# Kernel tuning notes

Measured on AMD Instinct MI355X. Metric: run time of the kernel, lower is better.

The kernel has to match this reference:

```python
import jax, jax.numpy as jnp
import numpy as np

N, D_IN, D_HID, D_Z = 8192, 512, 256, 64


def setup_inputs() -> dict:
    key = jax.random.key(0)
    k1, k2, k3, k4, k5 = jax.random.split(key, 5)
    x = jax.random.normal(k1, (N, D_IN), dtype=jnp.float32)
    adj = jax.random.uniform(k2, (N, N), dtype=jnp.float32)
    # Glorot-ish init for GCN weights
    W_hidden = jax.random.normal(k3, (D_IN, D_HID), dtype=jnp.float32) / np.sqrt(D_IN)
    W_mean = jax.random.normal(k4, (D_HID, D_Z), dtype=jnp.float32) / np.sqrt(D_HID)
    W_logstd = jax.random.normal(k5, (D_HID, D_Z), dtype=jnp.float32) / np.sqrt(D_HID)
    return {"x": x, "adj": adj, "W_hidden": W_hidden, "W_mean": W_mean, "W_logstd": W_logstd}


def _gcn(x, adj, W, act):
    # GraphConvolution (eval mode: dropout is identity): act(adj @ (x @ W))
    support = x @ W            # [N, out]
    out = adj @ support        # [N, out]  (sparse adj matmul in the original)
    return act(out)


def reference(x, adj, W_hidden, W_mean, W_logstd):
    hidden = _gcn(x, adj, W_hidden, jax.nn.relu)        # [N, hid]
    z_mean = _gcn(hidden, adj, W_mean, lambda t: t)     # [N, z]
    z_log_std = _gcn(hidden, adj, W_logstd, lambda t: t)
    # eval-mode reparameterize: z = z_mean
    z = z_mean
    # InnerProductDecoder with act = identity (as constructed in GCNModelVAE)
    recon = z @ z.T                                     # [N, N]
    return recon, z_mean, z_log_std
```

## Files before the change

### kernel.cpp

```cpp
#include <hip/hip_runtime.h>
#include <hip/hip_bf16.h>
#include <cstdint>


typedef __hip_bfloat16 hbf16;
typedef __bf16 bf16x8 __attribute__((ext_vector_type(8)));
typedef __bf16 bf16x4 __attribute__((ext_vector_type(4)));
typedef float  f32x4  __attribute__((ext_vector_type(4)));

#define N_NODES 8192
#define D_INF   512
#define D_HID   256
#define D_Z     64
#define KSPLIT  8

enum { EPI_NORM = 0, EPI_RELU = 1, EPI_TRANS = 2, EPI_SPLIT = 3 };

__device__ __forceinline__ float tofloat(float v) { return v; }
__device__ __forceinline__ float tofloat(hbf16 v) { return __bfloat162float(v); }

__device__ __forceinline__ bf16x8 load8(const hbf16* p) {
    return *(const bf16x8*)p;
}
__device__ __forceinline__ bf16x8 load8(const float* p) {
    f32x4 f0 = *(const f32x4*)p;
    f32x4 f1 = *(const f32x4*)(p + 4);
    bf16x8 r;
    r[0] = (__bf16)f0[0]; r[1] = (__bf16)f0[1];
    r[2] = (__bf16)f0[2]; r[3] = (__bf16)f0[3];
    r[4] = (__bf16)f1[0]; r[5] = (__bf16)f1[1];
    r[6] = (__bf16)f1[2]; r[7] = (__bf16)f1[3];
    return r;
}

__device__ __forceinline__ void store1(float* p, float v) { *p = v; }
__device__ __forceinline__ void store1(hbf16* p, float v) { *p = __float2bfloat16(v); }

__global__ void detect_dtype(const unsigned int* __restrict__ w, int* __restrict__ flag) {
    __shared__ int cnt;
    if (threadIdx.x == 0) cnt = 0;
    __syncthreads();
    int c = 0;
#pragma unroll
    for (int i = 0; i < 16; ++i) {
        unsigned int v = w[threadIdx.x * 16 + i];
        unsigned int lo = v & 0xFFFFu;
        if (lo != 0u && (lo >> 8) <= 0x3Fu) ++c;
    }
    atomicAdd(&cnt, c);
    __syncthreads();
    if (threadIdx.x == 0) *flag = (cnt > 2560) ? 1 : 0;
}

template <int EPI, int PIPE, typename TA, typename TOUT>
__global__ __launch_bounds__(256)
void gemm_nt64(const int* __restrict__ flag,
               const TA* __restrict__ A, int lda,
               const hbf16* __restrict__ B, int ldb,
               TOUT* __restrict__ C0, TOUT* __restrict__ C1,
               hbf16* __restrict__ CWS, int ldc, int K)
{
    if ((*flag != 0) != (PIPE != 0)) return;

    __shared__ hbf16 As[64 * 64];
    __shared__ hbf16 Bs[64 * 64];

    const int tid  = threadIdx.x;
    const int lane = tid & 63;
    const int w    = tid >> 6;
    const int wm0  = (w >> 1) * 32;
    const int wn0  = (w & 1) * 32;

    const int m0 = blockIdx.y * 64;
    const int n0 = blockIdx.x * 64;

    const int srow = tid >> 3;
    const int scol = (tid & 7) * 8;

    const size_t a_base = (size_t)(m0 + srow) * lda + scol;
    const size_t b_base = (size_t)(n0 + srow) * ldb + scol;

    f32x4 acc[2][2];
#pragma unroll
    for (int i = 0; i < 2; ++i)
#pragma unroll
        for (int j = 0; j < 2; ++j)
            acc[i][j] = (f32x4){0.f, 0.f, 0.f, 0.f};

    const int mrow = lane & 15;
    const int kq   = (lane >> 4) * 8;

    for (int k0 = 0; k0 < K; k0 += 64) {
        bf16x8 va0 = load8(A + a_base + k0);
        bf16x8 va1 = load8(A + a_base + (size_t)32 * lda + k0);
        bf16x8 vb0 = load8(B + b_base + k0);
        bf16x8 vb1 = load8(B + b_base + (size_t)32 * ldb + k0);

        __syncthreads();
        *(bf16x8*)&As[srow * 64 + scol]        = va0;
        *(bf16x8*)&As[(srow + 32) * 64 + scol] = va1;
        *(bf16x8*)&Bs[srow * 64 + scol]        = vb0;
        *(bf16x8*)&Bs[(srow + 32) * 64 + scol] = vb1;
        __syncthreads();

#pragma unroll
        for (int ks = 0; ks < 2; ++ks) {
            bf16x8 a0 = *(const bf16x8*)&As[(wm0 + mrow) * 64 + ks * 32 + kq];
            bf16x8 a1 = *(const bf16x8*)&As[(wm0 + 16 + mrow) * 64 + ks * 32 + kq];
            bf16x8 b0 = *(const bf16x8*)&Bs[(wn0 + mrow) * 64 + ks * 32 + kq];
            bf16x8 b1 = *(const bf16x8*)&Bs[(wn0 + 16 + mrow) * 64 + ks * 32 + kq];
            acc[0][0] = __builtin_amdgcn_mfma_f32_16x16x32_bf16(a0, b0, acc[0][0], 0, 0, 0);
            acc[0][1] = __builtin_amdgcn_mfma_f32_16x16x32_bf16(a0, b1, acc[0][1], 0, 0, 0);
            acc[1][0] = __builtin_amdgcn_mfma_f32_16x16x32_bf16(a1, b0, acc[1][0], 0, 0, 0);
            acc[1][1] = __builtin_amdgcn_mfma_f32_16x16x32_bf16(a1, b1, acc[1][1], 0, 0, 0);
        }
    }

    const int cn = lane & 15;
    const int rq = (lane >> 4) * 4;
#pragma unroll
    for (int mt = 0; mt < 2; ++mt)
#pragma unroll
        for (int nt = 0; nt < 2; ++nt)
#pragma unroll
            for (int r = 0; r < 4; ++r) {
                int row = m0 + wm0 + mt * 16 + rq + r;
                int col = n0 + wn0 + nt * 16 + cn;
                float v = acc[mt][nt][r];
                if (EPI == EPI_RELU) v = v > 0.f ? v : 0.f;
                if (EPI == EPI_TRANS) {
                    store1(&C0[(size_t)col * ldc + row], v);
                } else if (EPI == EPI_SPLIT) {
                    if (col < D_Z) {
                        store1(&C0[(size_t)row * D_Z + col], v);
                        CWS[(size_t)row * D_Z + col] = __float2bfloat16(v);
                    } else {
                        store1(&C1[(size_t)row * D_Z + (col - D_Z)], v);
                    }
                } else {
                    store1(&C0[(size_t)row * ldc + col], v);
                }
            }
}

template <int PIPE, int NBLK, typename TA>
__global__ __launch_bounds__(256)
void gemm_nt64_splitk(const int* __restrict__ flag,
                      const TA* __restrict__ A, int lda,
                      const hbf16* __restrict__ B, int ldb,
                      float* __restrict__ C, int ldc, int K)
{
    if ((*flag != 0) != (PIPE != 0)) return;

    __shared__ hbf16 As[64 * 64];
    __shared__ hbf16 Bs[64 * 64];

    const int q   = gridDim.x >> 3;
    const int lid = ((int)blockIdx.x & 7) * q + ((int)blockIdx.x >> 3);
    const int nb  = lid & (NBLK - 1);
    const int rem = lid / NBLK;
    const int mb  = rem & (N_NODES / 64 - 1);
    const int kb  = rem / (N_NODES / 64);

    const int tid  = threadIdx.x;
    const int lane = tid & 63;
    const int w    = tid >> 6;
    const int wm0  = (w >> 1) * 32;
    const int wn0  = (w & 1) * 32;

    const int m0 = mb * 64;
    const int n0 = nb * 64;

    const int srow = tid >> 3;
    const int scol = (tid & 7) * 8;

    const size_t a_base = (size_t)(m0 + srow) * lda + scol;
    const size_t b_base = (size_t)(n0 + srow) * ldb + scol;

    f32x4 acc[2][2];
#pragma unroll
    for (int i = 0; i < 2; ++i)
#pragma unroll
        for (int j = 0; j < 2; ++j)
            acc[i][j] = (f32x4){0.f, 0.f, 0.f, 0.f};

    const int mrow = lane & 15;
    const int kq   = (lane >> 4) * 8;

    const int kchunk = K / KSPLIT;
    const int k_lo   = kb * kchunk;
    const int k_hi   = k_lo + kchunk;

    for (int k0 = k_lo; k0 < k_hi; k0 += 64) {
        bf16x8 va0 = load8(A + a_base + k0);
        bf16x8 va1 = load8(A + a_base + (size_t)32 * lda + k0);
        bf16x8 vb0 = load8(B + b_base + k0);
        bf16x8 vb1 = load8(B + b_base + (size_t)32 * ldb + k0);

        __syncthreads();
        *(bf16x8*)&As[srow * 64 + scol]        = va0;
        *(bf16x8*)&As[(srow + 32) * 64 + scol] = va1;
        *(bf16x8*)&Bs[srow * 64 + scol]        = vb0;
        *(bf16x8*)&Bs[(srow + 32) * 64 + scol] = vb1;
        __syncthreads();

#pragma unroll
        for (int ks = 0; ks < 2; ++ks) {
            bf16x8 a0 = *(const bf16x8*)&As[(wm0 + mrow) * 64 + ks * 32 + kq];
            bf16x8 a1 = *(const bf16x8*)&As[(wm0 + 16 + mrow) * 64 + ks * 32 + kq];
            bf16x8 b0 = *(const bf16x8*)&Bs[(wn0 + mrow) * 64 + ks * 32 + kq];
            bf16x8 b1 = *(const bf16x8*)&Bs[(wn0 + 16 + mrow) * 64 + ks * 32 + kq];
            acc[0][0] = __builtin_amdgcn_mfma_f32_16x16x32_bf16(a0, b0, acc[0][0], 0, 0, 0);
            acc[0][1] = __builtin_amdgcn_mfma_f32_16x16x32_bf16(a0, b1, acc[0][1], 0, 0, 0);
            acc[1][0] = __builtin_amdgcn_mfma_f32_16x16x32_bf16(a1, b0, acc[1][0], 0, 0, 0);
            acc[1][1] = __builtin_amdgcn_mfma_f32_16x16x32_bf16(a1, b1, acc[1][1], 0, 0, 0);
        }
    }

    const int cn = lane & 15;
    const int rq = (lane >> 4) * 4;
#pragma unroll
    for (int mt = 0; mt < 2; ++mt)
#pragma unroll
        for (int nt = 0; nt < 2; ++nt)
#pragma unroll
            for (int r = 0; r < 4; ++r) {
                int row = m0 + wm0 + mt * 16 + rq + r;
                int col = n0 + wn0 + nt * 16 + cn;
                atomicAdd(&C[(size_t)row * ldc + col], acc[mt][nt][r]);
            }
}

__global__ void zero_f32(float* __restrict__ p, int n4) {
    int i = blockIdx.x * 256 + threadIdx.x;
    if (i < n4) ((f32x4*)p)[i] = (f32x4){0.f, 0.f, 0.f, 0.f};
}

template <int PIPE>
__global__ void epi_relu(const int* __restrict__ flag,
                         const float* __restrict__ S, hbf16* __restrict__ H) {
    if ((*flag != 0) != (PIPE != 0)) return;
    int i = blockIdx.x * 256 + threadIdx.x;
    f32x4 v = ((const f32x4*)S)[i];
    bf16x4 o;
#pragma unroll
    for (int j = 0; j < 4; ++j) {
        float f = v[j] > 0.f ? v[j] : 0.f;
        o[j] = (__bf16)f;
    }
    ((bf16x4*)H)[i] = o;
}

template <int PIPE, typename T>
__global__ void epi_split(const int* __restrict__ flag,
                          const float* __restrict__ Zc,
                          T* __restrict__ zmean, T* __restrict__ zlog,
                          hbf16* __restrict__ zws) {
    if ((*flag != 0) != (PIPE != 0)) return;
    int i = blockIdx.x * 256 + threadIdx.x;
    f32x4 v = ((const f32x4*)Zc)[i];
    int i4  = i << 2;
    int row = i4 >> 7;
    int col = i4 & 127;
    if (col < D_Z) {
        size_t o = (size_t)row * D_Z + col;
#pragma unroll
        for (int j = 0; j < 4; ++j) {
            store1(&zmean[o + j], v[j]);
            zws[o + j] = __float2bfloat16(v[j]);
        }
    } else {
        size_t o = (size_t)row * D_Z + (col - D_Z);
#pragma unroll
        for (int j = 0; j < 4; ++j) store1(&zlog[o + j], v[j]);
    }
}

template <int PIPE, typename T>
__global__ void prep_whT(const int* __restrict__ flag,
                         const T* __restrict__ W, hbf16* __restrict__ WT) {
    if ((*flag != 0) != (PIPE != 0)) return;
    int o = blockIdx.x * 256 + threadIdx.x;
    int n = o >> 9;
    int k = o & 511;
    WT[o] = __float2bfloat16(tofloat(W[k * D_HID + n]));
}

template <int PIPE, typename T>
__global__ void prep_wcT(const int* __restrict__ flag,
                         const T* __restrict__ Wm, const T* __restrict__ Wl,
                         hbf16* __restrict__ WcT) {
    if ((*flag != 0) != (PIPE != 0)) return;
    int o = blockIdx.x * 256 + threadIdx.x;
    int n = o >> 8;
    int k = o & 255;
    WcT[o] = __float2bfloat16(tofloat((n < D_Z) ? Wm[k * D_Z + n]
                                                : Wl[k * D_Z + (n - D_Z)]));
}

template <int PIPE, typename T>
static void launch_pipeline(void* const* d_in, void* d_out,
                            int* flag, hbf16* S1T, hbf16* H, hbf16* WhT,
                            hbf16* WcT, hbf16* TT, hbf16* ZmWS,
                            float* Hacc, float* Zc,
                            hipStream_t stream) {
    const T* x   = (const T*)d_in[0];
    const T* adj = (const T*)d_in[1];
    const T* Wh  = (const T*)d_in[2];
    const T* Wm  = (const T*)d_in[3];
    const T* Wl  = (const T*)d_in[4];

    T* recon = (T*)d_out;
    T* zmean = recon + (size_t)N_NODES * N_NODES;
    T* zlog  = zmean + (size_t)N_NODES * D_Z;

    prep_whT<PIPE, T><<<512, 256, 0, stream>>>(flag, Wh, WhT);
    prep_wcT<PIPE, T><<<128, 256, 0, stream>>>(flag, Wm, Wl, WcT);

    gemm_nt64<EPI_TRANS, PIPE, T, hbf16>
        <<<dim3(D_HID / 64, N_NODES / 64), 256, 0, stream>>>(
        flag, x, D_INF, WhT, D_INF, S1T, (hbf16*)nullptr, (hbf16*)nullptr,
        N_NODES, D_INF);

    gemm_nt64_splitk<PIPE, 4, T>
        <<<4 * (N_NODES / 64) * KSPLIT, 256, 0, stream>>>(
        flag, adj, N_NODES, S1T, N_NODES, Hacc, D_HID, N_NODES);
    epi_relu<PIPE><<<2048, 256, 0, stream>>>(flag, Hacc, H);

    gemm_nt64<EPI_TRANS, PIPE, hbf16, hbf16>
        <<<dim3(2 * D_Z / 64, N_NODES / 64), 256, 0, stream>>>(
        flag, H, D_HID, WcT, D_HID, TT, (hbf16*)nullptr, (hbf16*)nullptr,
        N_NODES, D_HID);

    gemm_nt64_splitk<PIPE, 2, T>
        <<<2 * (N_NODES / 64) * KSPLIT, 256, 0, stream>>>(
        flag, adj, N_NODES, TT, N_NODES, Zc, 2 * D_Z, N_NODES);
    epi_split<PIPE, T><<<1024, 256, 0, stream>>>(flag, Zc, zmean, zlog, ZmWS);

    gemm_nt64<EPI_NORM, PIPE, hbf16, T>
        <<<dim3(N_NODES / 64, N_NODES / 64), 256, 0, stream>>>(
        flag, ZmWS, D_Z, ZmWS, D_Z, recon, (T*)nullptr, (hbf16*)nullptr,
        N_NODES, D_Z);
}

extern "C" void kernel_launch(void* const* d_in, const int* in_sizes, int n_in,
                              void* d_out, int out_size, void* d_ws, size_t ws_size,
                              hipStream_t stream) {
    int*   flag = (int*)d_ws;
    hbf16* S1T  = (hbf16*)((char*)d_ws + 256);
    hbf16* H    = S1T + (size_t)D_HID * N_NODES;
    hbf16* WhT  = H   + (size_t)N_NODES * D_HID;
    hbf16* WcT  = WhT + (size_t)D_HID * D_INF;
    hbf16* TT   = WcT + (size_t)2 * D_Z * D_HID;
    hbf16* ZmWS = TT  + (size_t)2 * D_Z * N_NODES;
    float* Hacc = (float*)(ZmWS + (size_t)N_NODES * D_Z);
    float* Zc   = Hacc + (size_t)N_NODES * D_HID;

    detect_dtype<<<1, 256, 0, stream>>>((const unsigned int*)d_in[1], flag);

    zero_f32<<<3072, 256, 0, stream>>>(
        Hacc, (N_NODES * D_HID + N_NODES * 2 * D_Z) / 4);

    launch_pipeline<1, hbf16>(d_in, d_out, flag, S1T, H, WhT, WcT, TT, ZmWS,
                              Hacc, Zc, stream);
    launch_pipeline<0, float>(d_in, d_out, flag, S1T, H, WhT, WcT, TT, ZmWS,
                              Hacc, Zc, stream);
}
```

Before: 659.6 us.

## Widen split-K adjacency GEMM tile to 64x128 and XOR-swizzle LDS tiles

```diff
diff --git a/kernel.cpp b/kernel.cpp
--- a/kernel.cpp
+++ b/kernel.cpp
@@ -36,6 +36,13 @@
 __device__ __forceinline__ void store1(float* p, float v) { *p = v; }
 __device__ __forceinline__ void store1(hbf16* p, float v) { *p = __float2bfloat16(v); }
 
+__device__ __forceinline__ int swzoff(int row, int col) {
+    int byte = (row << 7) + (col << 1);
+    return byte ^ ((row & 7) << 4);
+}
+#define LDS8(base, row, col) (*(bf16x8*)((char*)(base) + swzoff((row), (col))))
+#define LDS8C(base, row, col) (*(const bf16x8*)((const char*)(base) + swzoff((row), (col))))
+
 __global__ void detect_dtype(const unsigned int* __restrict__ w, int* __restrict__ flag) {
     __shared__ int cnt;
     if (threadIdx.x == 0) cnt = 0;
@@ -97,18 +104,19 @@
         bf16x8 vb1 = load8(B + b_base + (size_t)32 * ldb + k0);
 
         __syncthreads();
-        *(bf16x8*)&As[srow * 64 + scol]        = va0;
-        *(bf16x8*)&As[(srow + 32) * 64 + scol] = va1;
-        *(bf16x8*)&Bs[srow * 64 + scol]        = vb0;
-        *(bf16x8*)&Bs[(srow + 32) * 64 + scol] = vb1;
+        LDS8(As, srow,      scol) = va0;
+        LDS8(As, srow + 32, scol) = va1;
+        LDS8(Bs, srow,      scol) = vb0;
+        LDS8(Bs, srow + 32, scol) = vb1;
         __syncthreads();
 
 #pragma unroll
         for (int ks = 0; ks < 2; ++ks) {
-            bf16x8 a0 = *(const bf16x8*)&As[(wm0 + mrow) * 64 + ks * 32 + kq];
-            bf16x8 a1 = *(const bf16x8*)&As[(wm0 + 16 + mrow) * 64 + ks * 32 + kq];
-            bf16x8 b0 = *(const bf16x8*)&Bs[(wn0 + mrow) * 64 + ks * 32 + kq];
-            bf16x8 b1 = *(const bf16x8*)&Bs[(wn0 + 16 + mrow) * 64 + ks * 32 + kq];
+            const int kc = ks * 32 + kq;
+            bf16x8 a0 = LDS8C(As, wm0 + mrow,      kc);
+            bf16x8 a1 = LDS8C(As, wm0 + 16 + mrow, kc);
+            bf16x8 b0 = LDS8C(Bs, wn0 + mrow,      kc);
+            bf16x8 b1 = LDS8C(Bs, wn0 + 16 + mrow, kc);
             acc[0][0] = __builtin_amdgcn_mfma_f32_16x16x32_bf16(a0, b0, acc[0][0], 0, 0, 0);
             acc[0][1] = __builtin_amdgcn_mfma_f32_16x16x32_bf16(a0, b1, acc[0][1], 0, 0, 0);
             acc[1][0] = __builtin_amdgcn_mfma_f32_16x16x32_bf16(a1, b0, acc[1][0], 0, 0, 0);
@@ -144,16 +152,16 @@
 }
 
 template <int PIPE, int NBLK, typename TA>
-__global__ __launch_bounds__(256)
-void gemm_nt64_splitk(const int* __restrict__ flag,
-                      const TA* __restrict__ A, int lda,
-                      const hbf16* __restrict__ B, int ldb,
-                      float* __restrict__ C, int ldc, int K)
+__global__ __launch_bounds__(256, 4)
+void gemm_nt128_splitk(const int* __restrict__ flag,
+                       const TA* __restrict__ A, int lda,
+                       const hbf16* __restrict__ B, int ldb,
+                       float* __restrict__ C, int ldc, int K)
 {
     if ((*flag != 0) != (PIPE != 0)) return;
 
     __shared__ hbf16 As[64 * 64];
-    __shared__ hbf16 Bs[64 * 64];
+    __shared__ hbf16 Bs[128 * 64];
 
     const int q   = gridDim.x >> 3;
     const int lid = ((int)blockIdx.x & 7) * q + ((int)blockIdx.x >> 3);
@@ -166,10 +174,10 @@
     const int lane = tid & 63;
     const int w    = tid >> 6;
     const int wm0  = (w >> 1) * 32;
-    const int wn0  = (w & 1) * 32;
+    const int wn0  = (w & 1) * 64;
 
     const int m0 = mb * 64;
-    const int n0 = nb * 64;
+    const int n0 = nb * 128;
 
     const int srow = tid >> 3;
     const int scol = (tid & 7) * 8;
@@ -177,11 +185,11 @@
     const size_t a_base = (size_t)(m0 + srow) * lda + scol;
     const size_t b_base = (size_t)(n0 + srow) * ldb + scol;
 
-    f32x4 acc[2][2];
+    f32x4 acc[2][4];
 #pragma unroll
     for (int i = 0; i < 2; ++i)
 #pragma unroll
-        for (int j = 0; j < 2; ++j)
+        for (int j = 0; j < 4; ++j)
             acc[i][j] = (f32x4){0.f, 0.f, 0.f, 0.f};
 
     const int mrow = lane & 15;
@@ -196,24 +204,29 @@
         bf16x8 va1 = load8(A + a_base + (size_t)32 * lda + k0);
         bf16x8 vb0 = load8(B + b_base + k0);
         bf16x8 vb1 = load8(B + b_base + (size_t)32 * ldb + k0);
+        bf16x8 vb2 = load8(B + b_base + (size_t)64 * ldb + k0);
+        bf16x8 vb3 = load8(B + b_base + (size_t)96 * ldb + k0);
 
         __syncthreads();
-        *(bf16x8*)&As[srow * 64 + scol]        = va0;
-        *(bf16x8*)&As[(srow + 32) * 64 + scol] = va1;
-        *(bf16x8*)&Bs[srow * 64 + scol]        = vb0;
-        *(bf16x8*)&Bs[(srow + 32) * 64 + scol] = vb1;
+        LDS8(As, srow,      scol) = va0;
+        LDS8(As, srow + 32, scol) = va1;
+        LDS8(Bs, srow,      scol) = vb0;
+        LDS8(Bs, srow + 32, scol) = vb1;
+        LDS8(Bs, srow + 64, scol) = vb2;
+        LDS8(Bs, srow + 96, scol) = vb3;
         __syncthreads();
 
 #pragma unroll
         for (int ks = 0; ks < 2; ++ks) {
-            bf16x8 a0 = *(const bf16x8*)&As[(wm0 + mrow) * 64 + ks * 32 + kq];
-            bf16x8 a1 = *(const bf16x8*)&As[(wm0 + 16 + mrow) * 64 + ks * 32 + kq];
-            bf16x8 b0 = *(const bf16x8*)&Bs[(wn0 + mrow) * 64 + ks * 32 + kq];
-            bf16x8 b1 = *(const bf16x8*)&Bs[(wn0 + 16 + mrow) * 64 + ks * 32 + kq];
-            acc[0][0] = __builtin_amdgcn_mfma_f32_16x16x32_bf16(a0, b0, acc[0][0], 0, 0, 0);
-            acc[0][1] = __builtin_amdgcn_mfma_f32_16x16x32_bf16(a0, b1, acc[0][1], 0, 0, 0);
-            acc[1][0] = __builtin_amdgcn_mfma_f32_16x16x32_bf16(a1, b0, acc[1][0], 0, 0, 0);
-            acc[1][1] = __builtin_amdgcn_mfma_f32_16x16x32_bf16(a1, b1, acc[1][1], 0, 0, 0);
+            const int kc = ks * 32 + kq;
+            bf16x8 a0 = LDS8C(As, wm0 + mrow,      kc);
+            bf16x8 a1 = LDS8C(As, wm0 + 16 + mrow, kc);
+#pragma unroll
+            for (int nt = 0; nt < 4; ++nt) {
+                bf16x8 b = LDS8C(Bs, wn0 + nt * 16 + mrow, kc);
+                acc[0][nt] = __builtin_amdgcn_mfma_f32_16x16x32_bf16(a0, b, acc[0][nt], 0, 0, 0);
+                acc[1][nt] = __builtin_amdgcn_mfma_f32_16x16x32_bf16(a1, b, acc[1][nt], 0, 0, 0);
+            }
         }
     }
 
@@ -222,7 +235,7 @@
 #pragma unroll
     for (int mt = 0; mt < 2; ++mt)
 #pragma unroll
-        for (int nt = 0; nt < 2; ++nt)
+        for (int nt = 0; nt < 4; ++nt)
 #pragma unroll
             for (int r = 0; r < 4; ++r) {
                 int row = m0 + wm0 + mt * 16 + rq + r;
@@ -322,8 +335,8 @@
         flag, x, D_INF, WhT, D_INF, S1T, (hbf16*)nullptr, (hbf16*)nullptr,
         N_NODES, D_INF);
 
-    gemm_nt64_splitk<PIPE, 4, T>
-        <<<4 * (N_NODES / 64) * KSPLIT, 256, 0, stream>>>(
+    gemm_nt128_splitk<PIPE, 2, T>
+        <<<2 * (N_NODES / 64) * KSPLIT, 256, 0, stream>>>(
         flag, adj, N_NODES, S1T, N_NODES, Hacc, D_HID, N_NODES);
     epi_relu<PIPE><<<2048, 256, 0, stream>>>(flag, Hacc, H);
 
@@ -332,8 +345,8 @@
         flag, H, D_HID, WcT, D_HID, TT, (hbf16*)nullptr, (hbf16*)nullptr,
         N_NODES, D_HID);
 
-    gemm_nt64_splitk<PIPE, 2, T>
-        <<<2 * (N_NODES / 64) * KSPLIT, 256, 0, stream>>>(
+    gemm_nt128_splitk<PIPE, 1, T>
+        <<<1 * (N_NODES / 64) * KSPLIT, 256, 0, stream>>>(
         flag, adj, N_NODES, TT, N_NODES, Zc, 2 * D_Z, N_NODES);
     epi_split<PIPE, T><<<1024, 256, 0, stream>>>(flag, Zc, zmean, zlog, ZmWS);
 
```

Result: faster. 611.5 us (-7.3%).
